# Optimization experiments

Measured on AMD Instinct MI355X. Metric: run time of the kernel, lower is better.

Reference implementation:

```python
import jax, jax.numpy as jnp
import numpy as np

N_HEADS = 16
K_CH = 1024 // N_HEADS  # 64
SCALE = 1.0 / np.sqrt(K_CH)


def setup_inputs() -> dict:
    key = jax.random.key(0)
    ks = jax.random.split(key, 10)
    B, C, T = 4, 1024, 2048
    Cout = 1024
    xavier = lambda k, o, i: jax.random.uniform(k, (o, i), jnp.float32, -1.0, 1.0) * np.sqrt(6.0 / (o + i))
    return {
        "x": jax.random.normal(ks[0], (B, C, T), jnp.float32),
        "c": jax.random.normal(ks[1], (B, C, T), jnp.float32),
        "Wq": xavier(ks[2], C, C), "bq": jnp.zeros((C,), jnp.float32),
        "Wk": xavier(ks[3], C, C), "bk": jnp.zeros((C,), jnp.float32),
        "Wv": xavier(ks[4], C, C), "bv": jnp.zeros((C,), jnp.float32),
        "Wo": xavier(ks[5], Cout, C), "bo": jnp.zeros((Cout,), jnp.float32),
    }


def reference(x, c, Wq, bq, Wk, bk, Wv, bv, Wo, bo):
    B, C, T = x.shape
    H, K = N_HEADS, K_CH
    # 1x1 Conv1d == per-timestep linear: [O,C] @ [B,C,T] -> [B,O,T]
    q = jnp.einsum('oc,bct->bot', Wq, x) + bq[None, :, None]
    k = jnp.einsum('oc,bct->bot', Wk, c) + bk[None, :, None]
    v = jnp.einsum('oc,bct->bot', Wv, c) + bv[None, :, None]
    # split heads: b (h k) t -> b h k t
    q = q.reshape(B, H, K, T)
    k = k.reshape(B, H, K, -1)
    v = v.reshape(B, H, K, -1)
    scores = jnp.einsum('bhkt,bhks->bhts', q, k) * SCALE  # [B,H,Tt,Ts]
    p = jax.nn.softmax(scores, axis=-1)
    out = jnp.einsum('bhts,bhks->bhkt', p, v)  # b h k t
    out = out.reshape(B, H * K, T)
    return jnp.einsum('oc,bct->bot', Wo, out) + bo[None, :, None]
```

## Files before the change

### kernel.cpp

```cpp
#include <hip/hip_runtime.h>
#include <stdint.h>

typedef __bf16 bf16x8 __attribute__((ext_vector_type(8)));
typedef float f32x4 __attribute__((ext_vector_type(4)));
typedef float f32x16 __attribute__((ext_vector_type(16)));
typedef unsigned u32x2 __attribute__((ext_vector_type(2)));
typedef unsigned u32x4 __attribute__((ext_vector_type(4)));

#define LOG2E 1.44269504088896340736f
#define ATT_SCALE 0.125f
#define CL (ATT_SCALE * LOG2E)
#define SWZ(row, colb) ((colb) ^ (((row) & 7) << 4))

#define GLOAD_LDS16(gp, lp)                                                  \
  __builtin_amdgcn_global_load_lds(                                          \
      (const __attribute__((address_space(1))) void*)(gp),                   \
      (__attribute__((address_space(3))) void*)(lp), 16, 0, 0)

__device__ __forceinline__ unsigned short f2bf(float f) {
  unsigned int x = __float_as_uint(f);
  x += 0x7fffu + ((x >> 16) & 1u);
  return (unsigned short)(x >> 16);
}

__device__ __forceinline__ float fexp2(float x) {
#if __has_builtin(__builtin_amdgcn_exp2f)
  return __builtin_amdgcn_exp2f(x);
#else
  return exp2f(x);
#endif
}

__device__ __forceinline__ unsigned cvtpk(float lo, float hi) {
  unsigned r;
  asm("v_cvt_pk_bf16_f32 %0, %1, %2" : "=v"(r) : "v"(lo), "v"(hi));
  return r;
}

__device__ __forceinline__ u32x2 plswap(unsigned a, unsigned b) {
#if __has_builtin(__builtin_amdgcn_permlane32_swap)
  return __builtin_amdgcn_permlane32_swap(a, b, false, false);
#else
  unsigned ax = (unsigned)__shfl_xor((int)a, 32);
  unsigned bx = (unsigned)__shfl_xor((int)b, 32);
  int hi = (threadIdx.x & 32) ? 1 : 0;
  u32x2 r;
  r[0] = hi ? bx : a;
  r[1] = hi ? b : ax;
  return r;
#endif
}

__global__ __launch_bounds__(256) void cvt_f32_bf16(const float* __restrict__ in,
                                                    unsigned short* __restrict__ out,
                                                    int n, float scale) {
  int i = (blockIdx.x * 256 + threadIdx.x) * 4;
  if (i >= n) return;
  float4 v = *(const float4*)(in + i);
  ushort4 o;
  o.x = f2bf(v.x * scale); o.y = f2bf(v.y * scale);
  o.z = f2bf(v.z * scale); o.w = f2bf(v.w * scale);
  *(ushort4*)(out + i) = o;
}

__global__ __launch_bounds__(256) void transpose_cvt(const float* __restrict__ in,
                                                     unsigned short* __restrict__ out,
                                                     int C, int T) {
  __shared__ unsigned short tile[32][33];
  int b = blockIdx.z;
  int t0 = blockIdx.x * 32, c0 = blockIdx.y * 32;
  int tx = threadIdx.x & 31, ty = threadIdx.x >> 5;
  const float* src = in + ((size_t)b * C + c0) * T + t0;
  #pragma unroll
  for (int i = 0; i < 4; ++i) {
    int cc = ty + i * 8;
    tile[cc][tx] = f2bf(src[(size_t)cc * T + tx]);
  }
  __syncthreads();
  unsigned short* dst = out + ((size_t)b * T + t0) * C + c0;
  #pragma unroll
  for (int i = 0; i < 4; ++i) {
    int tt = ty + i * 8;
    dst[(size_t)tt * C + tx] = tile[tx][tt];
  }
}

__global__ __launch_bounds__(256) void qkv_gemm(
    const unsigned short* __restrict__ xT, const unsigned short* __restrict__ cT,
    const unsigned short* __restrict__ wq, const unsigned short* __restrict__ wk,
    const unsigned short* __restrict__ wv,
    const float* __restrict__ bq, const float* __restrict__ bk,
    const float* __restrict__ bv,
    unsigned short* __restrict__ QT, unsigned short* __restrict__ KT,
    unsigned short* __restrict__ Vb) {
  __shared__ __align__(16) char lds[2 * 16384];
  char* As = lds;
  char* Bs = lds + 16384;
  const size_t sBT = (size_t)2048 * 1024;

  const int id = (blockIdx.x & 7) * 192 + (blockIdx.x >> 3);
  const int op = id >> 9;
  const int r = id & 511;
  const int z = r >> 7;
  const unsigned short *A, *Bw;
  unsigned short* Cp;
  const float* bias;
  int m0, n0, ldC, bias_is_m;
  float bs;
  if (op == 2) {
    n0 = (r & 15) * 128; m0 = ((r >> 4) & 7) * 128;
    A = wv; Bw = cT + z * sBT; Cp = Vb + z * (size_t)1024 * 2048;
    bias = bv; ldC = 2048; bias_is_m = 1; bs = 1.0f;
  } else {
    n0 = (r & 7) * 128; m0 = ((r >> 3) & 15) * 128;
    A = (op == 0 ? xT : cT) + z * sBT;
    Bw = (op == 0 ? wq : wk);
    Cp = (op == 0 ? QT : KT) + z * sBT;
    bias = (op == 0 ? bq : bk); ldC = 1024; bias_is_m = 0;
    bs = (op == 0) ? CL : 1.0f;
  }

  const int tid = threadIdx.x;
  const int l = tid & 63, w = tid >> 6;
  const int g = l >> 4, j = l & 15;
  const int wr = w >> 1, wc = w & 1;
  const int srow = tid >> 3, sslot = tid & 7;

  f32x4 acc[4][4] = {};

  for (int k0 = 0; k0 < 1024; k0 += 64) {
    __syncthreads();
    #pragma unroll
    for (int p = 0; p < 4; ++p) {
      int row = p * 32 + srow;
      int ch = sslot ^ (row & 7);
      GLOAD_LDS16(A + (size_t)(m0 + row) * 1024 + k0 + ch * 8, As + (p * 256 + tid) * 16);
      GLOAD_LDS16(Bw + (size_t)(n0 + row) * 1024 + k0 + ch * 8, Bs + (p * 256 + tid) * 16);
    }
    __syncthreads();
    #pragma unroll
    for (int k2 = 0; k2 < 2; ++k2) {
      bf16x8 af[4], bfr[4];
      #pragma unroll
      for (int mf = 0; mf < 4; ++mf) {
        int row = wr * 64 + mf * 16 + j;
        af[mf] = *(const bf16x8*)(As + row * 128 + SWZ(row, k2 * 64 + g * 16));
      }
      #pragma unroll
      for (int nf = 0; nf < 4; ++nf) {
        int row = wc * 64 + nf * 16 + j;
        bfr[nf] = *(const bf16x8*)(Bs + row * 128 + SWZ(row, k2 * 64 + g * 16));
      }
      #pragma unroll
      for (int mf = 0; mf < 4; ++mf)
        #pragma unroll
        for (int nf = 0; nf < 4; ++nf)
          acc[mf][nf] = __builtin_amdgcn_mfma_f32_16x16x32_bf16(af[mf], bfr[nf], acc[mf][nf], 0, 0, 0);
    }
  }

  #pragma unroll
  for (int mf = 0; mf < 4; ++mf) {
    #pragma unroll
    for (int rr = 0; rr < 4; ++rr) {
      int m = m0 + wr * 64 + mf * 16 + g * 4 + rr;
      float bm = bias_is_m ? bias[m] * bs : 0.f;
      #pragma unroll
      for (int nf = 0; nf < 4; ++nf) {
        int n = n0 + wc * 64 + nf * 16 + j;
        float val = acc[mf][nf][rr] + bm + (bias_is_m ? 0.f : bias[n] * bs);
        Cp[(size_t)m * ldC + n] = f2bf(val);
      }
    }
  }
}

__global__ __launch_bounds__(256) void gemm_out(
    const unsigned short* __restrict__ Wo, const unsigned short* __restrict__ OT,
    float* __restrict__ Out, const float* __restrict__ bias) {
  __shared__ __align__(16) char lds[2 * 16384];
  char* As = lds;
  char* Bs = lds + 16384;
  const size_t sBT = (size_t)2048 * 1024;
  const int z = blockIdx.z;
  const int m0 = blockIdx.y * 128, n0 = blockIdx.x * 128;
  const unsigned short* A = Wo;
  const unsigned short* B = OT + z * sBT;
  float* Cp = Out + z * (size_t)1024 * 2048;

  const int tid = threadIdx.x;
  const int l = tid & 63, w = tid >> 6;
  const int g = l >> 4, j = l & 15;
  const int wr = w >> 1, wc = w & 1;
  const int srow = tid >> 3, sslot = tid & 7;

  f32x4 acc[4][4] = {};

  for (int k0 = 0; k0 < 1024; k0 += 64) {
    __syncthreads();
    #pragma unroll
    for (int p = 0; p < 4; ++p) {
      int row = p * 32 + srow;
      int ch = sslot ^ (row & 7);
      GLOAD_LDS16(A + (size_t)(m0 + row) * 1024 + k0 + ch * 8, As + (p * 256 + tid) * 16);
      GLOAD_LDS16(B + (size_t)(n0 + row) * 1024 + k0 + ch * 8, Bs + (p * 256 + tid) * 16);
    }
    __syncthreads();
    #pragma unroll
    for (int k2 = 0; k2 < 2; ++k2) {
      bf16x8 af[4], bfr[4];
      #pragma unroll
      for (int mf = 0; mf < 4; ++mf) {
        int row = wr * 64 + mf * 16 + j;
        af[mf] = *(const bf16x8*)(As + row * 128 + SWZ(row, k2 * 64 + g * 16));
      }
      #pragma unroll
      for (int nf = 0; nf < 4; ++nf) {
        int row = wc * 64 + nf * 16 + j;
        bfr[nf] = *(const bf16x8*)(Bs + row * 128 + SWZ(row, k2 * 64 + g * 16));
      }
      #pragma unroll
      for (int mf = 0; mf < 4; ++mf)
        #pragma unroll
        for (int nf = 0; nf < 4; ++nf)
          acc[mf][nf] = __builtin_amdgcn_mfma_f32_16x16x32_bf16(af[mf], bfr[nf], acc[mf][nf], 0, 0, 0);
    }
  }

  #pragma unroll
  for (int mf = 0; mf < 4; ++mf) {
    #pragma unroll
    for (int rr = 0; rr < 4; ++rr) {
      int m = m0 + wr * 64 + mf * 16 + g * 4 + rr;
      float bm = bias[m];
      #pragma unroll
      for (int nf = 0; nf < 4; ++nf) {
        int n = n0 + wc * 64 + nf * 16 + j;
        Cp[(size_t)m * 2048 + n] = acc[mf][nf][rr] + bm;
      }
    }
  }
}

__global__ __launch_bounds__(256, 3) void attn_kernel3(const unsigned short* __restrict__ QT,
                                                       const unsigned short* __restrict__ KT,
                                                       const unsigned short* __restrict__ V,
                                                       unsigned short* __restrict__ OT) {
  __shared__ __align__(16) char Ks[8192];
  __shared__ __align__(16) char Vs[8192];
  __shared__ float lbuf[4][32];

  const int fid = blockIdx.x;
  const int xcd = fid & 7, idx = fid >> 3;
  const int bh = ((idx & 7) << 3) | xcd;
  const int tblk = idx >> 3;
  const int b = bh >> 4, h = bh & 15;

  const int tid = threadIdx.x;
  const int w = tid >> 6, l = tid & 63, lo5 = l & 31, hi = l >> 5;
  const int tq0 = tblk * 128 + w * 32;

  bf16x8 q[4];
  {
    const unsigned short* Qb = QT + ((size_t)(b * 2048 + tq0 + lo5)) * 1024 + h * 64 + hi * 8;
    #pragma unroll
    for (int kb = 0; kb < 4; ++kb) q[kb] = *(const bf16x8*)(Qb + kb * 16);
  }

  f32x16 o[2] = {};
  float lr = 0.f;

  const int srow0 = tid >> 3, sslot = tid & 7;
  const unsigned short* Kg0 = KT + ((size_t)b * 2048) * 1024 + h * 64;
  const unsigned short* Vg0 = V + ((size_t)(b * 1024 + h * 64)) * 2048;

  for (int s0 = 0; s0 < 2048; s0 += 64) {
    __syncthreads();
    #pragma unroll
    for (int p = 0; p < 2; ++p) {
      int row = p * 32 + srow0;
      int ch = sslot ^ (row & 7);
      GLOAD_LDS16(Kg0 + (size_t)(s0 + row) * 1024 + ch * 8, Ks + (p * 256 + tid) * 16);
      GLOAD_LDS16(Vg0 + (size_t)row * 2048 + s0 + ch * 8, Vs + (p * 256 + tid) * 16);
    }
    __syncthreads();

    f32x16 p0 = {}, p1 = {};
    #pragma unroll
    for (int kb = 0; kb < 4; ++kb) {
      int r0 = lo5, r1 = 32 + lo5;
      bf16x8 ka0 = *(const bf16x8*)(Ks + r0 * 128 + SWZ(r0, kb * 32 + hi * 16));
      bf16x8 ka1 = *(const bf16x8*)(Ks + r1 * 128 + SWZ(r1, kb * 32 + hi * 16));
      p0 = __builtin_amdgcn_mfma_f32_32x32x16_bf16(ka0, q[kb], p0, 0, 0, 0);
      p1 = __builtin_amdgcn_mfma_f32_32x32x16_bf16(ka1, q[kb], p1, 0, 0, 0);
    }

    float ls0 = 0.f, ls1 = 0.f, ls2 = 0.f, ls3 = 0.f;
    #pragma unroll
    for (int r = 0; r < 16; r += 4) {
      float e0 = fexp2(p0[r]), e1 = fexp2(p0[r + 1]), e2 = fexp2(p0[r + 2]), e3 = fexp2(p0[r + 3]);
      p0[r] = e0; p0[r + 1] = e1; p0[r + 2] = e2; p0[r + 3] = e3;
      ls0 += e0; ls1 += e1; ls2 += e2; ls3 += e3;
    }
    #pragma unroll
    for (int r = 0; r < 16; r += 4) {
      float e0 = fexp2(p1[r]), e1 = fexp2(p1[r + 1]), e2 = fexp2(p1[r + 2]), e3 = fexp2(p1[r + 3]);
      p1[r] = e0; p1[r + 1] = e1; p1[r + 2] = e2; p1[r + 3] = e3;
      ls0 += e0; ls1 += e1; ls2 += e2; ls3 += e3;
    }
    lr += (ls0 + ls1) + (ls2 + ls3);

    u32x4 pa[4];
    {
      u32x2 ra = plswap(cvtpk(p0[0], p0[1]), cvtpk(p0[4], p0[5]));
      u32x2 rb = plswap(cvtpk(p0[2], p0[3]), cvtpk(p0[6], p0[7]));
      pa[0] = (u32x4){ra[0], rb[0], ra[1], rb[1]};
      u32x2 rc = plswap(cvtpk(p0[8], p0[9]), cvtpk(p0[12], p0[13]));
      u32x2 rd = plswap(cvtpk(p0[10], p0[11]), cvtpk(p0[14], p0[15]));
      pa[1] = (u32x4){rc[0], rd[0], rc[1], rd[1]};
      u32x2 re = plswap(cvtpk(p1[0], p1[1]), cvtpk(p1[4], p1[5]));
      u32x2 rf = plswap(cvtpk(p1[2], p1[3]), cvtpk(p1[6], p1[7]));
      pa[2] = (u32x4){re[0], rf[0], re[1], rf[1]};
      u32x2 rg = plswap(cvtpk(p1[8], p1[9]), cvtpk(p1[12], p1[13]));
      u32x2 rh = plswap(cvtpk(p1[10], p1[11]), cvtpk(p1[14], p1[15]));
      pa[3] = (u32x4){rg[0], rh[0], rg[1], rh[1]};
    }

    #pragma unroll
    for (int sb = 0; sb < 4; ++sb)
      #pragma unroll
      for (int kb2 = 0; kb2 < 2; ++kb2) {
        int row = kb2 * 32 + lo5;
        bf16x8 vb = *(const bf16x8*)(Vs + row * 128 + SWZ(row, sb * 32 + hi * 16));
        o[kb2] = __builtin_amdgcn_mfma_f32_32x32x16_bf16(
            __builtin_bit_cast(bf16x8, pa[sb]), vb, o[kb2], 0, 0, 0);
      }
  }

  u32x2 sw = plswap(__float_as_uint(lr), __float_as_uint(lr));
  float lt = __uint_as_float(sw[0]) + __uint_as_float(sw[1]);
  if (hi == 0) lbuf[w][lo5] = 1.0f / lt;
  unsigned short* Ob = OT + ((size_t)(b * 2048 + tq0)) * 1024 + h * 64 + lo5;
  #pragma unroll
  for (int r = 0; r < 16; ++r) {
    int srow = (r & 3) + 8 * (r >> 2) + 4 * hi;
    float inv = lbuf[w][srow];
    Ob[(size_t)srow * 1024 + 0]  = f2bf(o[0][r] * inv);
    Ob[(size_t)srow * 1024 + 32] = f2bf(o[1][r] * inv);
  }
}

extern "C" void kernel_launch(void* const* d_in, const int* in_sizes, int n_in,
                              void* d_out, int out_size, void* d_ws, size_t ws_size,
                              hipStream_t stream) {
  const float* x  = (const float*)d_in[0];
  const float* c  = (const float*)d_in[1];
  const float* Wq = (const float*)d_in[2];
  const float* bq = (const float*)d_in[3];
  const float* Wk = (const float*)d_in[4];
  const float* bk = (const float*)d_in[5];
  const float* Wv = (const float*)d_in[6];
  const float* bv = (const float*)d_in[7];
  const float* Wo = (const float*)d_in[8];
  const float* bo = (const float*)d_in[9];

  const size_t MB = 1024 * 1024;
  char* ws = (char*)d_ws;
  unsigned short* wqb = (unsigned short*)(ws + 0 * MB);
  unsigned short* wkb = (unsigned short*)(ws + 2 * MB);
  unsigned short* wvb = (unsigned short*)(ws + 4 * MB);
  unsigned short* wob = (unsigned short*)(ws + 6 * MB);
  unsigned short* xT  = (unsigned short*)(ws + 8 * MB);
  unsigned short* cT  = (unsigned short*)(ws + 24 * MB);
  unsigned short* QT  = (unsigned short*)(ws + 40 * MB);
  unsigned short* KT  = (unsigned short*)(ws + 56 * MB);
  unsigned short* Vb  = (unsigned short*)(ws + 72 * MB);
  unsigned short* OT  = xT;

  cvt_f32_bf16<<<1024, 256, 0, stream>>>(Wq, wqb, 1 << 20, CL);
  cvt_f32_bf16<<<1024, 256, 0, stream>>>(Wk, wkb, 1 << 20, 1.0f);
  cvt_f32_bf16<<<1024, 256, 0, stream>>>(Wv, wvb, 1 << 20, 1.0f);
  cvt_f32_bf16<<<1024, 256, 0, stream>>>(Wo, wob, 1 << 20, 1.0f);
  transpose_cvt<<<dim3(64, 32, 4), 256, 0, stream>>>(x, xT, 1024, 2048);
  transpose_cvt<<<dim3(64, 32, 4), 256, 0, stream>>>(c, cT, 1024, 2048);

  qkv_gemm<<<dim3(1536), 256, 0, stream>>>(xT, cT, wqb, wkb, wvb, bq, bk, bv, QT, KT, Vb);

  attn_kernel3<<<dim3(1024), 256, 0, stream>>>(QT, KT, Vb, OT);

  gemm_out<<<dim3(16, 8, 4), 256, 0, stream>>>(wob, OT, (float*)d_out, bo);
}
```

Before: 222.0 us.

## Double-buffer LDS in GEMMs and attention, merge conversion kernel launches

The QKV GEMM, output GEMM and attention kernel now keep two LDS buffers and prefetch the next k/s tile with global_load_lds while computing on the current one, with one barrier per iteration instead of two. This aims to hide global-to-LDS latency behind MFMA work. The four weight-conversion launches become one kernel, and the two transposes become one, which cuts launch overhead. The cost is double the LDS per block (64KB for the GEMMs, 32KB for attention), which may lower occupancy. The prefetch also relies on the single end-of-iteration barrier to order the async loads safely.

```diff
diff --git a/kernel.cpp b/kernel.cpp
--- a/kernel.cpp
+++ b/kernel.cpp
@@ -51,11 +51,16 @@
 #endif
 }
 
-__global__ __launch_bounds__(256) void cvt_f32_bf16(const float* __restrict__ in,
-                                                    unsigned short* __restrict__ out,
-                                                    int n, float scale) {
-  int i = (blockIdx.x * 256 + threadIdx.x) * 4;
-  if (i >= n) return;
+__global__ __launch_bounds__(256) void cvt_weights(
+    const float* __restrict__ w0, const float* __restrict__ w1,
+    const float* __restrict__ w2, const float* __restrict__ w3,
+    unsigned short* __restrict__ o0, unsigned short* __restrict__ o1,
+    unsigned short* __restrict__ o2, unsigned short* __restrict__ o3) {
+  int sel = blockIdx.x >> 10;
+  const float* in = sel == 0 ? w0 : sel == 1 ? w1 : sel == 2 ? w2 : w3;
+  unsigned short* out = sel == 0 ? o0 : sel == 1 ? o1 : sel == 2 ? o2 : o3;
+  float scale = sel == 0 ? CL : 1.0f;
+  int i = ((blockIdx.x & 1023) * 256 + threadIdx.x) * 4;
   float4 v = *(const float4*)(in + i);
   ushort4 o;
   o.x = f2bf(v.x * scale); o.y = f2bf(v.y * scale);
@@ -63,11 +68,16 @@
   *(ushort4*)(out + i) = o;
 }
 
-__global__ __launch_bounds__(256) void transpose_cvt(const float* __restrict__ in,
-                                                     unsigned short* __restrict__ out,
-                                                     int C, int T) {
+__global__ __launch_bounds__(256) void transpose_cvt2(const float* __restrict__ x,
+                                                      const float* __restrict__ c,
+                                                      unsigned short* __restrict__ xT,
+                                                      unsigned short* __restrict__ cT) {
   __shared__ unsigned short tile[32][33];
-  int b = blockIdx.z;
+  const int C = 1024, T = 2048;
+  int z = blockIdx.z;
+  const float* in = (z < 4) ? x : c;
+  unsigned short* out = (z < 4) ? xT : cT;
+  int b = z & 3;
   int t0 = blockIdx.x * 32, c0 = blockIdx.y * 32;
   int tx = threadIdx.x & 31, ty = threadIdx.x >> 5;
   const float* src = in + ((size_t)b * C + c0) * T + t0;
@@ -93,9 +103,7 @@
     const float* __restrict__ bv,
     unsigned short* __restrict__ QT, unsigned short* __restrict__ KT,
     unsigned short* __restrict__ Vb) {
-  __shared__ __align__(16) char lds[2 * 16384];
-  char* As = lds;
-  char* Bs = lds + 16384;
+  __shared__ __align__(16) char lds[2][32768];
   const size_t sBT = (size_t)2048 * 1024;
 
   const int id = (blockIdx.x & 7) * 192 + (blockIdx.x >> 3);
@@ -128,8 +136,9 @@
 
   f32x4 acc[4][4] = {};
 
-  for (int k0 = 0; k0 < 1024; k0 += 64) {
-    __syncthreads();
+  auto stage = [&](int bsel, int k0) {
+    char* As = lds[bsel];
+    char* Bs = lds[bsel] + 16384;
     #pragma unroll
     for (int p = 0; p < 4; ++p) {
       int row = p * 32 + srow;
@@ -137,7 +146,16 @@
       GLOAD_LDS16(A + (size_t)(m0 + row) * 1024 + k0 + ch * 8, As + (p * 256 + tid) * 16);
       GLOAD_LDS16(Bw + (size_t)(n0 + row) * 1024 + k0 + ch * 8, Bs + (p * 256 + tid) * 16);
     }
-    __syncthreads();
+  };
+
+  stage(0, 0);
+  __syncthreads();
+
+  for (int t = 0; t < 16; ++t) {
+    int cur = t & 1;
+    if (t < 15) stage(cur ^ 1, (t + 1) * 64);
+    char* As = lds[cur];
+    char* Bs = lds[cur] + 16384;
     #pragma unroll
     for (int k2 = 0; k2 < 2; ++k2) {
       bf16x8 af[4], bfr[4];
@@ -157,6 +175,7 @@
         for (int nf = 0; nf < 4; ++nf)
           acc[mf][nf] = __builtin_amdgcn_mfma_f32_16x16x32_bf16(af[mf], bfr[nf], acc[mf][nf], 0, 0, 0);
     }
+    __syncthreads();
   }
 
   #pragma unroll
@@ -178,9 +197,7 @@
 __global__ __launch_bounds__(256) void gemm_out(
     const unsigned short* __restrict__ Wo, const unsigned short* __restrict__ OT,
     float* __restrict__ Out, const float* __restrict__ bias) {
-  __shared__ __align__(16) char lds[2 * 16384];
-  char* As = lds;
-  char* Bs = lds + 16384;
+  __shared__ __align__(16) char lds[2][32768];
   const size_t sBT = (size_t)2048 * 1024;
   const int z = blockIdx.z;
   const int m0 = blockIdx.y * 128, n0 = blockIdx.x * 128;
@@ -196,8 +213,9 @@
 
   f32x4 acc[4][4] = {};
 
-  for (int k0 = 0; k0 < 1024; k0 += 64) {
-    __syncthreads();
+  auto stage = [&](int bsel, int k0) {
+    char* As = lds[bsel];
+    char* Bs = lds[bsel] + 16384;
     #pragma unroll
     for (int p = 0; p < 4; ++p) {
       int row = p * 32 + srow;
@@ -205,7 +223,16 @@
       GLOAD_LDS16(A + (size_t)(m0 + row) * 1024 + k0 + ch * 8, As + (p * 256 + tid) * 16);
       GLOAD_LDS16(B + (size_t)(n0 + row) * 1024 + k0 + ch * 8, Bs + (p * 256 + tid) * 16);
     }
-    __syncthreads();
+  };
+
+  stage(0, 0);
+  __syncthreads();
+
+  for (int t = 0; t < 16; ++t) {
+    int cur = t & 1;
+    if (t < 15) stage(cur ^ 1, (t + 1) * 64);
+    char* As = lds[cur];
+    char* Bs = lds[cur] + 16384;
     #pragma unroll
     for (int k2 = 0; k2 < 2; ++k2) {
       bf16x8 af[4], bfr[4];
@@ -225,6 +252,7 @@
         for (int nf = 0; nf < 4; ++nf)
           acc[mf][nf] = __builtin_amdgcn_mfma_f32_16x16x32_bf16(af[mf], bfr[nf], acc[mf][nf], 0, 0, 0);
     }
+    __syncthreads();
   }
 
   #pragma unroll
@@ -242,12 +270,11 @@
   }
 }
 
-__global__ __launch_bounds__(256, 3) void attn_kernel3(const unsigned short* __restrict__ QT,
+__global__ __launch_bounds__(256, 3) void attn_kernel4(const unsigned short* __restrict__ QT,
                                                        const unsigned short* __restrict__ KT,
                                                        const unsigned short* __restrict__ V,
                                                        unsigned short* __restrict__ OT) {
-  __shared__ __align__(16) char Ks[8192];
-  __shared__ __align__(16) char Vs[8192];
+  __shared__ __align__(16) char kv[2][16384];
   __shared__ float lbuf[4][32];
 
   const int fid = blockIdx.x;
@@ -274,8 +301,9 @@
   const unsigned short* Kg0 = KT + ((size_t)b * 2048) * 1024 + h * 64;
   const unsigned short* Vg0 = V + ((size_t)(b * 1024 + h * 64)) * 2048;
 
-  for (int s0 = 0; s0 < 2048; s0 += 64) {
-    __syncthreads();
+  auto stage = [&](int bsel, int s0) {
+    char* Ks = kv[bsel];
+    char* Vs = kv[bsel] + 8192;
     #pragma unroll
     for (int p = 0; p < 2; ++p) {
       int row = p * 32 + srow0;
@@ -283,7 +311,16 @@
       GLOAD_LDS16(Kg0 + (size_t)(s0 + row) * 1024 + ch * 8, Ks + (p * 256 + tid) * 16);
       GLOAD_LDS16(Vg0 + (size_t)row * 2048 + s0 + ch * 8, Vs + (p * 256 + tid) * 16);
     }
-    __syncthreads();
+  };
+
+  stage(0, 0);
+  __syncthreads();
+
+  for (int t = 0; t < 32; ++t) {
+    int cur = t & 1;
+    if (t < 31) stage(cur ^ 1, (t + 1) * 64);
+    char* Ks = kv[cur];
+    char* Vs = kv[cur] + 8192;
 
     f32x16 p0 = {}, p1 = {};
     #pragma unroll
@@ -335,6 +372,7 @@
         o[kb2] = __builtin_amdgcn_mfma_f32_32x32x16_bf16(
             __builtin_bit_cast(bf16x8, pa[sb]), vb, o[kb2], 0, 0, 0);
       }
+    __syncthreads();
   }
 
   u32x2 sw = plswap(__float_as_uint(lr), __float_as_uint(lr));
@@ -377,16 +415,12 @@
   unsigned short* Vb  = (unsigned short*)(ws + 72 * MB);
   unsigned short* OT  = xT;
 
-  cvt_f32_bf16<<<1024, 256, 0, stream>>>(Wq, wqb, 1 << 20, CL);
-  cvt_f32_bf16<<<1024, 256, 0, stream>>>(Wk, wkb, 1 << 20, 1.0f);
-  cvt_f32_bf16<<<1024, 256, 0, stream>>>(Wv, wvb, 1 << 20, 1.0f);
-  cvt_f32_bf16<<<1024, 256, 0, stream>>>(Wo, wob, 1 << 20, 1.0f);
-  transpose_cvt<<<dim3(64, 32, 4), 256, 0, stream>>>(x, xT, 1024, 2048);
-  transpose_cvt<<<dim3(64, 32, 4), 256, 0, stream>>>(c, cT, 1024, 2048);
+  cvt_weights<<<dim3(4096), 256, 0, stream>>>(Wq, Wk, Wv, Wo, wqb, wkb, wvb, wob);
+  transpose_cvt2<<<dim3(64, 32, 8), 256, 0, stream>>>(x, c, xT, cT);
 
   qkv_gemm<<<dim3(1536), 256, 0, stream>>>(xT, cT, wqb, wkb, wvb, bq, bk, bv, QT, KT, Vb);
 
-  attn_kernel3<<<dim3(1024), 256, 0, stream>>>(QT, KT, Vb, OT);
+  attn_kernel4<<<dim3(1024), 256, 0, stream>>>(QT, KT, Vb, OT);
 
   gemm_out<<<dim3(16, 8, 4), 256, 0, stream>>>(wob, OT, (float*)d_out, bo);
 }
```

After: 205.8 us. 7.3% less time.
